# Kernel tuning notes

Measured on AMD Instinct MI355X. Metric: run time of the kernel, lower is better.

The kernel has to match this reference:

```python
import jax, jax.numpy as jnp
import numpy as np

B, T, F, M = 8, 512, 513, 8  # batch, time frames, freq bins, mics
AVERAGE = True
# upper-triangular mic pair indices (static)
_IU0, _IU1 = np.triu_indices(M)
IU0 = jnp.asarray(_IU0)
IU1 = jnp.asarray(_IU1)


def setup_inputs() -> dict:
    key = jax.random.key(0)
    Xs = jax.random.normal(key, (B, T, F, 2, M), dtype=jnp.float32)
    return {"Xs": Xs}


def reference(Xs):
    # Xs: [B, T, F, 2, M]
    re = Xs[..., 0, :]  # [B, T, F, M]
    im = Xs[..., 1, :]  # [B, T, F, M]
    # Only the upper-triangular entries of the rank-1 outer products are needed;
    # compute them directly (same math as matmul + triu gather, no MxM temp).
    re_i, re_j = re[..., IU0], re[..., IU1]  # [B, T, F, P]
    im_i, im_j = im[..., IU0], im[..., IU1]
    XXs_re = re_i * re_j + im_i * im_j
    XXs_im = re_i * im_j - im_i * re_j
    XXs = jnp.stack((XXs_re, XXs_im), axis=3)  # [B, T, F, 2, P]
    if AVERAGE:
        mean = jnp.mean(XXs, axis=1, keepdims=True)  # [B, 1, F, 2, P]
        XXs = jnp.broadcast_to(mean, XXs.shape)      # repeat over time
    return XXs
```

## Files before the change

kernel.cpp:

```cpp
#include <hip/hip_runtime.h>

constexpr int kB  = 8;
constexpr int kT  = 512;
constexpr int kF  = 513;
constexpr int kM  = 8;
constexpr int kNP = 36;
constexpr int kC  = 2 * kNP;
constexpr int kFT = 64;
constexpr int kNFT = 9;
constexpr int kNTC = 16;
constexpr int kTC = kT / kNTC;
constexpr int kLDP = kC + 1;
constexpr int kS4 = kF * kC / 4;
constexpr unsigned kBreg4 = (unsigned)kT * kS4;

__global__ __launch_bounds__(256) void cov_partial(const float* __restrict__ in,
                                                   float* __restrict__ out) {
  const int bx = blockIdx.x;
  const int b  = bx / (kNFT * kNTC);
  const int r  = bx - b * (kNFT * kNTC);
  const int ft = r / kNTC;
  const int tc = r - ft * kNTC;
  const int tid  = threadIdx.x;
  const int wave = tid >> 6;
  const int lane = tid & 63;
  const int f = ft * kFT + lane;

  float accR[kNP], accI[kNP];
#pragma unroll
  for (int p = 0; p < kNP; ++p) { accR[p] = 0.0f; accI[p] = 0.0f; }

  if (f < kF) {
    const int t0 = tc * kTC + wave;
    const float* base = in + ((size_t)(b * kT + t0) * kF + f) * (2 * kM);
    const size_t tstep = (size_t)4 * kF * (2 * kM);
#pragma unroll 2
    for (int it = 0; it < kTC / 4; ++it) {
      const float* ptr = base + it * tstep;
      const float4 r0 = *(const float4*)(ptr + 0);
      const float4 r1 = *(const float4*)(ptr + 4);
      const float4 i0 = *(const float4*)(ptr + 8);
      const float4 i1 = *(const float4*)(ptr + 12);
      const float re[kM] = {r0.x, r0.y, r0.z, r0.w, r1.x, r1.y, r1.z, r1.w};
      const float im[kM] = {i0.x, i0.y, i0.z, i0.w, i1.x, i1.y, i1.z, i1.w};
      int p = 0;
#pragma unroll
      for (int i = 0; i < kM; ++i) {
#pragma unroll
        for (int j = i; j < kM; ++j) {
          accR[p] += re[i] * re[j] + im[i] * im[j];
          accI[p] += re[i] * im[j] - im[i] * re[j];
          ++p;
        }
      }
    }
  }

  __shared__ float buf[2][kFT * kLDP];
  float* my = buf[wave & 1] + lane * kLDP;
  if (wave < 2) {
#pragma unroll
    for (int p = 0; p < kNP; ++p) { my[p] = accR[p]; my[kNP + p] = accI[p]; }
  }
  __syncthreads();
  if (wave >= 2) {
#pragma unroll
    for (int p = 0; p < kNP; ++p) { my[p] += accR[p]; my[kNP + p] += accI[p]; }
  }
  __syncthreads();

  const int nf = min(kFT, kF - ft * kFT);
  float* dst = out + ((size_t)(b * kT + (1 + tc)) * kF + ft * kFT) * kC;
  const int n = nf * kC;
  for (int e = tid; e < n; e += 256) {
    const int l = (unsigned)e / (unsigned)kC;
    const int p = e - l * kC;
    dst[e] = buf[0][l * kLDP + p] + buf[1][l * kLDP + p];
  }
}

__global__ __launch_bounds__(256) void cov_combine(float4* __restrict__ out) {
  const int total4 = kB * kS4;
  const int idx = blockIdx.x * 256 + threadIdx.x;
  if (idx >= total4) return;
  const int b = (unsigned)idx / (unsigned)kS4;
  const int fr4 = idx - b * kS4;
  const size_t bbase = (size_t)b * kBreg4;
  float4 s = make_float4(0.f, 0.f, 0.f, 0.f);
#pragma unroll
  for (int k = 0; k < kNTC; ++k) {
    const float4 v = out[bbase + (size_t)(1 + k) * kS4 + fr4];
    s.x += v.x; s.y += v.y; s.z += v.z; s.w += v.w;
  }
  const float sc = 1.0f / kT;
  s.x *= sc; s.y *= sc; s.z *= sc; s.w *= sc;
  out[bbase + fr4] = s;
}

__global__ __launch_bounds__(256) void cov_bcast(float4* __restrict__ out) {
  const unsigned total4 = (unsigned)kB * kT * kF * (kC / 4);
  const unsigned idx = blockIdx.x * 256u + threadIdx.x;
  if (idx >= total4) return;
  const unsigned g = idx / (kC / 4);
  const unsigned r = idx - g * (kC / 4);
  const unsigned b = g / (unsigned)(kT * kF);
  const unsigned f = g % (unsigned)kF;
  const unsigned src = (b * (unsigned)(kT * kF) + f) * (kC / 4) + r;
  out[idx] = out[src];
}

extern "C" void kernel_launch(void* const* d_in, const int* in_sizes, int n_in,
                              void* d_out, int out_size, void* d_ws, size_t ws_size,
                              hipStream_t stream) {
  const float* in = (const float*)d_in[0];
  float* out = (float*)d_out;

  cov_partial<<<dim3(kB * kNFT * kNTC), dim3(256), 0, stream>>>(in, out);

  const int total4 = kB * kS4;
  cov_combine<<<dim3((total4 + 255) / 256), dim3(256), 0, stream>>>((float4*)out);

  const unsigned total4b = (unsigned)kB * kT * kF * (kC / 4);
  cov_bcast<<<dim3((total4b + 255u) / 256u), dim3(256), 0, stream>>>((float4*)out);
}
```

Baseline: 149.7 us.

## Fuse partial, combine and broadcast kernels into one persistent kernel with grid barriers

Merges the three separate launches (per-time-chunk partial sums, combine/mean, broadcast over time) into a single kernel. The phases are separated by a software grid barrier built on atomics in the workspace, which is zeroed with a memset before the launch. The broadcast phase becomes a grid-stride loop with incrementally updated indices instead of a per-element division. The number of time chunks is also halved (16 to 8), so each block does more accumulation and the combine reads fewer partials. The goal is to remove inter-kernel launch gaps and tail effects. In exchange it adds barrier spin overhead, an extra memset, and a dependence on all 576 blocks being co-resident.

```diff
diff --git a/kernel.cpp b/kernel.cpp
--- a/kernel.cpp
+++ b/kernel.cpp
@@ -8,105 +8,150 @@
 constexpr int kC  = 2 * kNP;
 constexpr int kFT = 64;
 constexpr int kNFT = 9;
-constexpr int kNTC = 16;
-constexpr int kTC = kT / kNTC;
+constexpr int kNTC = 8;
+constexpr int kTC  = kT / kNTC;
 constexpr int kLDP = kC + 1;
-constexpr int kS4 = kF * kC / 4;
-constexpr unsigned kBreg4 = (unsigned)kT * kS4;
+constexpr int kS4  = kF * kC / 4;
+constexpr unsigned kBreg4  = (unsigned)kT * kS4;
+constexpr unsigned kTotal4 = (unsigned)kB * kBreg4;
+constexpr int kGrid    = kB * kNFT * kNTC;
+constexpr int kThreads = kGrid * 256;
+constexpr int kSweeps  = (int)((kTotal4 + kThreads - 1) / kThreads);
+constexpr unsigned kGStep = (unsigned)kThreads / 18u;
+constexpr unsigned kTF    = (unsigned)kT * kF;
+constexpr unsigned kFStep = kGStep % (unsigned)kF;
 
-__global__ __launch_bounds__(256) void cov_partial(const float* __restrict__ in,
-                                                   float* __restrict__ out) {
-  const int bx = blockIdx.x;
-  const int b  = bx / (kNFT * kNTC);
-  const int r  = bx - b * (kNFT * kNTC);
-  const int ft = r / kNTC;
-  const int tc = r - ft * kNTC;
+__device__ __forceinline__ void gridbar(unsigned* bar, unsigned nb) {
+  __syncthreads();
+  if (threadIdx.x == 0) {
+    __threadfence();
+    unsigned g = __hip_atomic_load(&bar[1], __ATOMIC_RELAXED,
+                                   __HIP_MEMORY_SCOPE_AGENT);
+    unsigned old = __hip_atomic_fetch_add(&bar[0], 1u, __ATOMIC_ACQ_REL,
+                                          __HIP_MEMORY_SCOPE_AGENT);
+    if (old == nb - 1u) {
+      __hip_atomic_store(&bar[0], 0u, __ATOMIC_RELAXED,
+                         __HIP_MEMORY_SCOPE_AGENT);
+      __hip_atomic_fetch_add(&bar[1], 1u, __ATOMIC_RELEASE,
+                             __HIP_MEMORY_SCOPE_AGENT);
+    } else {
+      while (__hip_atomic_load(&bar[1], __ATOMIC_ACQUIRE,
+                               __HIP_MEMORY_SCOPE_AGENT) == g) {
+        __builtin_amdgcn_s_sleep(2);
+      }
+    }
+  }
+  __syncthreads();
+}
+
+__global__ __launch_bounds__(256, 4)
+void cov_fused(const float* __restrict__ in, float* __restrict__ out,
+               unsigned* __restrict__ bar) {
   const int tid  = threadIdx.x;
   const int wave = tid >> 6;
   const int lane = tid & 63;
-  const int f = ft * kFT + lane;
+  float4* __restrict__ out4 = (float4*)out;
 
-  float accR[kNP], accI[kNP];
+  {
+    const int bx = blockIdx.x;
+    const int b  = bx / (kNFT * kNTC);
+    const int r  = bx - b * (kNFT * kNTC);
+    const int ft = r / kNTC;
+    const int tc = r - ft * kNTC;
+    const int f  = ft * kFT + lane;
+
+    float accR[kNP], accI[kNP];
 #pragma unroll
-  for (int p = 0; p < kNP; ++p) { accR[p] = 0.0f; accI[p] = 0.0f; }
+    for (int p = 0; p < kNP; ++p) { accR[p] = 0.0f; accI[p] = 0.0f; }
 
-  if (f < kF) {
-    const int t0 = tc * kTC + wave;
-    const float* base = in + ((size_t)(b * kT + t0) * kF + f) * (2 * kM);
-    const size_t tstep = (size_t)4 * kF * (2 * kM);
-#pragma unroll 2
-    for (int it = 0; it < kTC / 4; ++it) {
-      const float* ptr = base + it * tstep;
-      const float4 r0 = *(const float4*)(ptr + 0);
-      const float4 r1 = *(const float4*)(ptr + 4);
-      const float4 i0 = *(const float4*)(ptr + 8);
-      const float4 i1 = *(const float4*)(ptr + 12);
-      const float re[kM] = {r0.x, r0.y, r0.z, r0.w, r1.x, r1.y, r1.z, r1.w};
-      const float im[kM] = {i0.x, i0.y, i0.z, i0.w, i1.x, i1.y, i1.z, i1.w};
-      int p = 0;
+    if (f < kF) {
+      const int t0 = tc * kTC + wave;
+      const float* base = in + ((size_t)(b * kT + t0) * kF + f) * (2 * kM);
+      const size_t tstep = (size_t)4 * kF * (2 * kM);
+      for (int it = 0; it < kTC / 4; ++it) {
+        const float* ptr = base + it * tstep;
+        const float4 r0 = *(const float4*)(ptr + 0);
+        const float4 r1 = *(const float4*)(ptr + 4);
+        const float4 i0 = *(const float4*)(ptr + 8);
+        const float4 i1 = *(const float4*)(ptr + 12);
+        const float re[kM] = {r0.x, r0.y, r0.z, r0.w, r1.x, r1.y, r1.z, r1.w};
+        const float im[kM] = {i0.x, i0.y, i0.z, i0.w, i1.x, i1.y, i1.z, i1.w};
+        int p = 0;
 #pragma unroll
-      for (int i = 0; i < kM; ++i) {
+        for (int i = 0; i < kM; ++i) {
 #pragma unroll
-        for (int j = i; j < kM; ++j) {
-          accR[p] += re[i] * re[j] + im[i] * im[j];
-          accI[p] += re[i] * im[j] - im[i] * re[j];
-          ++p;
+          for (int j = i; j < kM; ++j) {
+            accR[p] += re[i] * re[j] + im[i] * im[j];
+            accI[p] += re[i] * im[j] - im[i] * re[j];
+            ++p;
+          }
         }
       }
     }
+
+    __shared__ float buf[2][kFT * kLDP];
+    float* my = buf[wave & 1] + lane * kLDP;
+    if (wave < 2) {
+#pragma unroll
+      for (int p = 0; p < kNP; ++p) { my[p] = accR[p]; my[kNP + p] = accI[p]; }
+    }
+    __syncthreads();
+    if (wave >= 2) {
+#pragma unroll
+      for (int p = 0; p < kNP; ++p) { my[p] += accR[p]; my[kNP + p] += accI[p]; }
+    }
+    __syncthreads();
+
+    const int nf = min(kFT, kF - ft * kFT);
+    float* dst = out + ((size_t)(b * kT + (1 + tc)) * kF + ft * kFT) * kC;
+    const int n = nf * kC;
+    for (int e = tid; e < n; e += 256) {
+      const int l = (unsigned)e / (unsigned)kC;
+      const int p = e - l * kC;
+      dst[e] = buf[0][l * kLDP + p] + buf[1][l * kLDP + p];
+    }
   }
 
-  __shared__ float buf[2][kFT * kLDP];
-  float* my = buf[wave & 1] + lane * kLDP;
-  if (wave < 2) {
+  gridbar(bar, (unsigned)gridDim.x);
+
+  {
+    const unsigned idx0 = blockIdx.x * 256u + (unsigned)tid;
+    if (idx0 < (unsigned)(kB * kS4)) {
+      const unsigned b2 = idx0 / (unsigned)kS4;
+      const unsigned fr = idx0 - b2 * (unsigned)kS4;
+      const size_t base = (size_t)b2 * kBreg4;
+      float4 s = make_float4(0.f, 0.f, 0.f, 0.f);
 #pragma unroll
-    for (int p = 0; p < kNP; ++p) { my[p] = accR[p]; my[kNP + p] = accI[p]; }
+      for (int k = 0; k < kNTC; ++k) {
+        const float4 v = out4[base + (size_t)(1 + k) * kS4 + fr];
+        s.x += v.x; s.y += v.y; s.z += v.z; s.w += v.w;
+      }
+      const float sc = 1.0f / kT;
+      s.x *= sc; s.y *= sc; s.z *= sc; s.w *= sc;
+      out4[base + fr] = s;
+    }
   }
-  __syncthreads();
-  if (wave >= 2) {
-#pragma unroll
-    for (int p = 0; p < kNP; ++p) { my[p] += accR[p]; my[kNP + p] += accI[p]; }
+
+  gridbar(bar, (unsigned)gridDim.x);
+
+  {
+    const unsigned idx0 = blockIdx.x * 256u + (unsigned)tid;
+    const unsigned r = idx0 % 18u;
+    const unsigned g0 = idx0 / 18u;
+    unsigned gb = g0;
+    unsigned f  = g0 % (unsigned)kF;
+    size_t srcb = 0;
+    size_t dst  = idx0;
+#pragma unroll 4
+    for (int k = 0; k < kSweeps; ++k) {
+      if (dst < (size_t)kTotal4)
+        out4[dst] = out4[srcb + (size_t)f * 18u + r];
+      dst += (size_t)kThreads;
+      gb += kGStep;
+      if (gb >= kTF) { gb -= kTF; srcb += kBreg4; }
+      f += kFStep; if (f >= (unsigned)kF) f -= (unsigned)kF;
+    }
   }
-  __syncthreads();
-
-  const int nf = min(kFT, kF - ft * kFT);
-  float* dst = out + ((size_t)(b * kT + (1 + tc)) * kF + ft * kFT) * kC;
-  const int n = nf * kC;
-  for (int e = tid; e < n; e += 256) {
-    const int l = (unsigned)e / (unsigned)kC;
-    const int p = e - l * kC;
-    dst[e] = buf[0][l * kLDP + p] + buf[1][l * kLDP + p];
-  }
-}
-
-__global__ __launch_bounds__(256) void cov_combine(float4* __restrict__ out) {
-  const int total4 = kB * kS4;
-  const int idx = blockIdx.x * 256 + threadIdx.x;
-  if (idx >= total4) return;
-  const int b = (unsigned)idx / (unsigned)kS4;
-  const int fr4 = idx - b * kS4;
-  const size_t bbase = (size_t)b * kBreg4;
-  float4 s = make_float4(0.f, 0.f, 0.f, 0.f);
-#pragma unroll
-  for (int k = 0; k < kNTC; ++k) {
-    const float4 v = out[bbase + (size_t)(1 + k) * kS4 + fr4];
-    s.x += v.x; s.y += v.y; s.z += v.z; s.w += v.w;
-  }
-  const float sc = 1.0f / kT;
-  s.x *= sc; s.y *= sc; s.z *= sc; s.w *= sc;
-  out[bbase + fr4] = s;
-}
-
-__global__ __launch_bounds__(256) void cov_bcast(float4* __restrict__ out) {
-  const unsigned total4 = (unsigned)kB * kT * kF * (kC / 4);
-  const unsigned idx = blockIdx.x * 256u + threadIdx.x;
-  if (idx >= total4) return;
-  const unsigned g = idx / (kC / 4);
-  const unsigned r = idx - g * (kC / 4);
-  const unsigned b = g / (unsigned)(kT * kF);
-  const unsigned f = g % (unsigned)kF;
-  const unsigned src = (b * (unsigned)(kT * kF) + f) * (kC / 4) + r;
-  out[idx] = out[src];
 }
 
 extern "C" void kernel_launch(void* const* d_in, const int* in_sizes, int n_in,
@@ -114,12 +159,8 @@
                               hipStream_t stream) {
   const float* in = (const float*)d_in[0];
   float* out = (float*)d_out;
+  unsigned* bar = (unsigned*)d_ws;
 
-  cov_partial<<<dim3(kB * kNFT * kNTC), dim3(256), 0, stream>>>(in, out);
-
-  const int total4 = kB * kS4;
-  cov_combine<<<dim3((total4 + 255) / 256), dim3(256), 0, stream>>>((float4*)out);
-
-  const unsigned total4b = (unsigned)kB * kT * kF * (kC / 4);
-  cov_bcast<<<dim3((total4b + 255u) / 256u), dim3(256), 0, stream>>>((float4*)out);
+  hipMemsetAsync(d_ws, 0, 2 * sizeof(unsigned), stream);
+  cov_fused<<<dim3(kGrid), dim3(256), 0, stream>>>(in, out, bar);
 }
```

New measurement: 425.3 us. 2.84x slower.
